# Optimization experiments

Measured on AMD Instinct MI355X. Metric: run time of the kernel, lower is better.

The kernel has to match this reference:

```python
import jax, jax.numpy as jnp
import numpy as np

B, A, D, REL, H = 8, 192, 128, 5, 128

def setup_inputs() -> dict:
    key = jax.random.key(0)
    ks = jax.random.split(key, 10)
    coord = jax.random.normal(ks[0], (B, A, D), jnp.float32)
    goal = jax.random.normal(ks[1], (B, A, D), jnp.float32)
    frontier = jax.random.normal(ks[2], (B, A, D), jnp.float32)
    rel_feat = jax.random.normal(ks[3], (B, A, A, REL), jnp.float32)
    rule_adj = jax.random.randint(ks[4], (B, A, A), 0, 2) > 0
    base_score = jax.random.normal(ks[5], (B, A, A), jnp.float32)
    graph_context = jax.random.normal(ks[6], (B, D), jnp.float32)
    fan_in = 6 * D + REL + D
    W1 = jax.random.normal(ks[7], (fan_in, H), jnp.float32) / np.sqrt(fan_in)
    b1 = jnp.zeros((H,), jnp.float32)
    W2 = jax.random.normal(ks[8], (H, 1), jnp.float32) / np.sqrt(H)
    b2 = jnp.zeros((1,), jnp.float32)
    return {"coord": coord, "goal": goal, "frontier": frontier, "rel_feat": rel_feat,
            "rule_adj": rule_adj, "base_score": base_score, "graph_context": graph_context,
            "W1": W1, "b1": b1, "W2": W2, "b2": b2}

def reference(coord, goal, frontier, rel_feat, rule_adj, base_score, graph_context, W1, b1, W2, b2):
    b, a, d = coord.shape
    def pair(x):
        xi = jnp.broadcast_to(x[:, :, None, :], (b, a, a, d))
        xj = jnp.broadcast_to(x[:, None, :, :], (b, a, a, d))
        return xi, xj
    ci, cj = pair(coord)
    gi, gj = pair(goal)
    fi, fj = pair(frontier)
    gc = jnp.broadcast_to(graph_context[:, None, None, :], (b, a, a, d))
    edge_in = jnp.concatenate([ci, cj, gi, gj, fi, fj, rel_feat, gc], axis=-1)  # [B,A,A,7D+rel]
    h = jax.nn.relu(edge_in @ W1 + b1)
    learned = (h @ W2 + b2)[..., 0]  # [B,A,A]
    score = base_score + learned
    score = jnp.where(rule_adj, score, jnp.float32(-1e9))
    weights = jax.nn.softmax(score, axis=-1)
    weights = weights * rule_adj.astype(weights.dtype)
    weights = weights / (weights.sum(axis=-1, keepdims=True) + 1e-8)
    return weights, score, learned
```

## Files before the change

kernel.cpp:

```cpp
#include <hip/hip_runtime.h>
#include <math.h>

#define NB 8
#define NA 192
#define ND 128
#define NREL 5
#define NH 128
#define ROWS 6
#define NPBLK ((NB * NA) / ROWS)

__global__ __launch_bounds__(256) void precompute_P(
    const float* __restrict__ coord, const float* __restrict__ goal,
    const float* __restrict__ frontier, const float* __restrict__ gctx,
    const float* __restrict__ W1, const float* __restrict__ b1,
    float* __restrict__ Pi, float* __restrict__ PjT, float* __restrict__ Gc)
{
    const int blk = blockIdx.x;
    const int tid = threadIdx.x;

    if (blk >= NPBLK) {
        __shared__ float red[256];
        const int b = blk - NPBLK;
        const int h = tid & 127, part = tid >> 7;
        const float* g = gctx + b * ND + part * 64;
        const float* w = W1 + (size_t)(6 * ND + NREL + part * 64) * NH + h;
        float acc = 0.f;
#pragma unroll 8
        for (int d = 0; d < 64; ++d) acc += g[d] * w[d * NH];
        red[tid] = acc;
        __syncthreads();
        if (part == 0) Gc[b * NH + h] = red[h] + red[h + 128] + b1[h];
        return;
    }

    __shared__ __align__(16) float X[ROWS][3 * ND];
    const int r0 = blk * ROWS;

    for (int idx = tid; idx < ROWS * 3 * ND; idx += 256) {
        int r = idx / (3 * ND);
        int k = idx % (3 * ND);
        int s = k >> 7, d = k & 127;
        const float* src = (s == 0) ? coord : (s == 1) ? goal : frontier;
        X[r][k] = src[(r0 + r) * ND + d];
    }
    __syncthreads();

    const int colLocal = tid & 127;
    const int role = tid >> 7;
    const int roleOff = role * 128;

    float acc[ROWS];
#pragma unroll
    for (int r = 0; r < ROWS; r++) acc[r] = 0.f;

    for (int s = 0; s < 3; ++s) {
        const float* wb = W1 + (size_t)(256 * s + roleOff) * NH + colLocal;
#pragma unroll 2
        for (int d = 0; d < ND; d += 4) {
            float w0 = wb[(d + 0) * NH];
            float w1 = wb[(d + 1) * NH];
            float w2 = wb[(d + 2) * NH];
            float w3 = wb[(d + 3) * NH];
#pragma unroll
            for (int r = 0; r < ROWS; r++) {
                float4 x = *(const float4*)&X[r][s * ND + d];
                acc[r] += x.x * w0 + x.y * w1 + x.z * w2 + x.w * w3;
            }
        }
    }

#pragma unroll
    for (int r = 0; r < ROWS; r++) {
        int row = r0 + r;
        if (role == 0) {
            Pi[(size_t)row * NH + colLocal] = acc[r];
        } else {
            int b = row / NA, a = row % NA;
            PjT[((size_t)b * NH + colLocal) * NA + a] = acc[r];
        }
    }
}

__global__ __launch_bounds__(192) void edge_kernel(
    const float* __restrict__ Pi, const float* __restrict__ PjT,
    const float* __restrict__ Gc, const float* __restrict__ W1,
    const float* __restrict__ W2, const float* __restrict__ b2v,
    const float* __restrict__ rel_feat, const int* __restrict__ rule_adj,
    const float* __restrict__ base_score,
    float* __restrict__ out_w, float* __restrict__ out_s, float* __restrict__ out_l)
{
    const int bi = blockIdx.x;
    const int b = bi / NA;
    const int tid = threadIdx.x;

    __shared__ float4 su1[NH];
    __shared__ float4 su2[NH];
    __shared__ float redA[3], redB[3], redC[3];

    if (tid < NH) {
        float pig = Pi[(size_t)bi * NH + tid] + Gc[b * NH + tid];
        const float* wr = W1 + (size_t)(6 * ND) * NH + tid;
        su1[tid] = make_float4(pig, wr[0 * NH], wr[1 * NH], wr[2 * NH]);
        su2[tid] = make_float4(wr[3 * NH], wr[4 * NH], W2[tid], 0.f);
    }

    float rel[NREL];
    const float* rf = rel_feat + ((size_t)bi * NA + tid) * NREL;
#pragma unroll
    for (int r = 0; r < NREL; r++) rel[r] = rf[r];

    __syncthreads();

    const float* pj = PjT + (size_t)b * NH * NA + tid;
    float acc = 0.f;
#pragma unroll 4
    for (int h = 0; h < NH; ++h) {
        float p = pj[h * NA];
        float4 a = su1[h];
        float4 c = su2[h];
        float pre = a.x + p;
        pre += rel[0] * a.y;
        pre += rel[1] * a.z;
        pre += rel[2] * a.w;
        pre += rel[3] * c.x;
        pre += rel[4] * c.y;
        acc += fmaxf(pre, 0.f) * c.z;
    }
    float learned = acc + b2v[0];
    out_l[(size_t)bi * NA + tid] = learned;

    const int adj = rule_adj[(size_t)bi * NA + tid];
    const float sc = adj ? (base_score[(size_t)bi * NA + tid] + learned) : -1e9f;
    out_s[(size_t)bi * NA + tid] = sc;

    const int wave = tid >> 6, lane = tid & 63;

    float m = sc;
#pragma unroll
    for (int off = 32; off > 0; off >>= 1) m = fmaxf(m, __shfl_xor(m, off, 64));
    if (lane == 0) redA[wave] = m;
    __syncthreads();
    m = fmaxf(fmaxf(redA[0], redA[1]), redA[2]);

    float e = __expf(sc - m);
    float S = e;
#pragma unroll
    for (int off = 32; off > 0; off >>= 1) S += __shfl_xor(S, off, 64);
    if (lane == 0) redB[wave] = S;
    __syncthreads();
    S = redB[0] + redB[1] + redB[2];

    float wj = adj ? e * (1.f / S) : 0.f;
    float sw = wj;
#pragma unroll
    for (int off = 32; off > 0; off >>= 1) sw += __shfl_xor(sw, off, 64);
    if (lane == 0) redC[wave] = sw;
    __syncthreads();
    sw = redC[0] + redC[1] + redC[2];

    out_w[(size_t)bi * NA + tid] = wj * (1.f / (sw + 1e-8f));
}

extern "C" void kernel_launch(void* const* d_in, const int* in_sizes, int n_in,
                              void* d_out, int out_size, void* d_ws, size_t ws_size,
                              hipStream_t stream) {
    const float* coord    = (const float*)d_in[0];
    const float* goal     = (const float*)d_in[1];
    const float* frontier = (const float*)d_in[2];
    const float* rel_feat = (const float*)d_in[3];
    const int*   rule_adj = (const int*)d_in[4];
    const float* base_sc  = (const float*)d_in[5];
    const float* gctx     = (const float*)d_in[6];
    const float* W1       = (const float*)d_in[7];
    const float* b1       = (const float*)d_in[8];
    const float* W2       = (const float*)d_in[9];
    const float* b2       = (const float*)d_in[10];

    float* Pi  = (float*)d_ws;
    float* PjT = Pi + NB * NA * NH;
    float* Gc  = PjT + NB * NH * NA;

    float* out_w = (float*)d_out;
    float* out_s = out_w + NB * NA * NA;
    float* out_l = out_s + NB * NA * NA;

    precompute_P<<<NPBLK + NB, 256, 0, stream>>>(coord, goal, frontier, gctx,
                                                 W1, b1, Pi, PjT, Gc);
    edge_kernel<<<NB * NA, 192, 0, stream>>>(Pi, PjT, Gc, W1, W2, b2, rel_feat,
                                             rule_adj, base_sc, out_w, out_s, out_l);
}
```

Measured before the change: 122.7 us.

## Split precompute K dimension across two blocks and sum partials in edge kernel

The precompute kernel now splits the 384-wide reduction over coord/goal/frontier into two halves, each handled by its own block. This doubles the block count from 256 to 512 so more of the GPU is used. The partial results are written to doubled workspace buffers and summed in the edge kernel. The cost is extra global reads in the edge kernel's inner h loop (two PjT loads per step) and twice the workspace traffic.

Result: faster. 116.8 us (-4.8%).

```diff
diff --git a/kernel.cpp b/kernel.cpp
--- a/kernel.cpp
+++ b/kernel.cpp
@@ -7,20 +7,21 @@
 #define NREL 5
 #define NH 128
 #define ROWS 6
-#define NPBLK ((NB * NA) / ROWS)
-
-__global__ __launch_bounds__(256) void precompute_P(
+#define NROWBLK ((NB * NA) / ROWS)
+#define NPBLK (NROWBLK * 2)
+
+__global__ __launch_bounds__(256, 4) void precompute_P(
     const float* __restrict__ coord, const float* __restrict__ goal,
     const float* __restrict__ frontier, const float* __restrict__ gctx,
     const float* __restrict__ W1, const float* __restrict__ b1,
-    float* __restrict__ Pi, float* __restrict__ PjT, float* __restrict__ Gc)
+    float* __restrict__ PiP, float* __restrict__ PjTP, float* __restrict__ Gc)
 {
     const int blk = blockIdx.x;
     const int tid = threadIdx.x;
 
-    if (blk >= NPBLK) {
+    if (blk >= 2 * NROWBLK) {
         __shared__ float red[256];
-        const int b = blk - NPBLK;
+        const int b = blk - 2 * NROWBLK;
         const int h = tid & 127, part = tid >> 7;
         const float* g = gctx + b * ND + part * 64;
         const float* w = W1 + (size_t)(6 * ND + NREL + part * 64) * NH + h;
@@ -33,15 +34,19 @@
         return;
     }
 
-    __shared__ __align__(16) float X[ROWS][3 * ND];
-    const int r0 = blk * ROWS;
-
-    for (int idx = tid; idx < ROWS * 3 * ND; idx += 256) {
-        int r = idx / (3 * ND);
-        int k = idx % (3 * ND);
+    const int rb = blk >> 1;
+    const int kh = blk & 1;
+    const int r0 = rb * ROWS;
+
+    __shared__ __align__(16) float X[ROWS][192];
+
+    for (int idx = tid; idx < ROWS * 192; idx += 256) {
+        int r = idx / 192;
+        int kk = idx - r * 192;
+        int k = kh * 192 + kk;
         int s = k >> 7, d = k & 127;
         const float* src = (s == 0) ? coord : (s == 1) ? goal : frontier;
-        X[r][k] = src[(r0 + r) * ND + d];
+        X[r][kk] = src[(r0 + r) * ND + d];
     }
     __syncthreads();
 
@@ -53,36 +58,39 @@
 #pragma unroll
     for (int r = 0; r < ROWS; r++) acc[r] = 0.f;
 
-    for (int s = 0; s < 3; ++s) {
-        const float* wb = W1 + (size_t)(256 * s + roleOff) * NH + colLocal;
-#pragma unroll 2
-        for (int d = 0; d < ND; d += 4) {
-            float w0 = wb[(d + 0) * NH];
-            float w1 = wb[(d + 1) * NH];
-            float w2 = wb[(d + 2) * NH];
-            float w3 = wb[(d + 3) * NH];
+    auto seg = [&](int kkStart, int sChunk, int dStart, int len) {
+        const float* wb = W1 + (size_t)(sChunk * 256 + roleOff + dStart) * NH + colLocal;
+#pragma unroll 4
+        for (int t = 0; t < len; t += 4) {
+            float w0 = wb[0 * NH];
+            float w1 = wb[1 * NH];
+            float w2 = wb[2 * NH];
+            float w3 = wb[3 * NH];
+            wb += 4 * NH;
 #pragma unroll
             for (int r = 0; r < ROWS; r++) {
-                float4 x = *(const float4*)&X[r][s * ND + d];
+                float4 x = *(const float4*)&X[r][kkStart + t];
                 acc[r] += x.x * w0 + x.y * w1 + x.z * w2 + x.w * w3;
             }
         }
-    }
+    };
+    if (kh == 0) { seg(0, 0, 0, 128); seg(128, 1, 0, 64); }
+    else         { seg(0, 1, 64, 64); seg(64, 2, 0, 128); }
 
 #pragma unroll
     for (int r = 0; r < ROWS; r++) {
         int row = r0 + r;
         if (role == 0) {
-            Pi[(size_t)row * NH + colLocal] = acc[r];
+            PiP[((size_t)kh * NB * NA + row) * NH + colLocal] = acc[r];
         } else {
-            int b = row / NA, a = row % NA;
-            PjT[((size_t)b * NH + colLocal) * NA + a] = acc[r];
+            int b = row / NA, a = row - b * NA;
+            PjTP[(((size_t)kh * NB + b) * NH + colLocal) * NA + a] = acc[r];
         }
     }
 }
 
 __global__ __launch_bounds__(192) void edge_kernel(
-    const float* __restrict__ Pi, const float* __restrict__ PjT,
+    const float* __restrict__ PiP, const float* __restrict__ PjTP,
     const float* __restrict__ Gc, const float* __restrict__ W1,
     const float* __restrict__ W2, const float* __restrict__ b2v,
     const float* __restrict__ rel_feat, const int* __restrict__ rule_adj,
@@ -98,7 +106,9 @@
     __shared__ float redA[3], redB[3], redC[3];
 
     if (tid < NH) {
-        float pig = Pi[(size_t)bi * NH + tid] + Gc[b * NH + tid];
+        float pig = PiP[(size_t)bi * NH + tid]
+                  + PiP[(size_t)(NB * NA + bi) * NH + tid]
+                  + Gc[b * NH + tid];
         const float* wr = W1 + (size_t)(6 * ND) * NH + tid;
         su1[tid] = make_float4(pig, wr[0 * NH], wr[1 * NH], wr[2 * NH]);
         su2[tid] = make_float4(wr[3 * NH], wr[4 * NH], W2[tid], 0.f);
@@ -111,11 +121,12 @@
 
     __syncthreads();
 
-    const float* pj = PjT + (size_t)b * NH * NA + tid;
+    const float* pj0 = PjTP + (size_t)b * NH * NA + tid;
+    const float* pj1 = pj0 + (size_t)NB * NH * NA;
     float acc = 0.f;
-#pragma unroll 4
+#pragma unroll 8
     for (int h = 0; h < NH; ++h) {
-        float p = pj[h * NA];
+        float p = pj0[h * NA] + pj1[h * NA];
         float4 a = su1[h];
         float4 c = su2[h];
         float pre = a.x + p;
@@ -176,16 +187,16 @@
     const float* W2       = (const float*)d_in[9];
     const float* b2       = (const float*)d_in[10];
 
-    float* Pi  = (float*)d_ws;
-    float* PjT = Pi + NB * NA * NH;
-    float* Gc  = PjT + NB * NH * NA;
+    float* PiP  = (float*)d_ws;
+    float* PjTP = PiP + 2 * NB * NA * NH;
+    float* Gc   = PjTP + 2 * NB * NH * NA;
 
     float* out_w = (float*)d_out;
     float* out_s = out_w + NB * NA * NA;
     float* out_l = out_s + NB * NA * NA;
 
-    precompute_P<<<NPBLK + NB, 256, 0, stream>>>(coord, goal, frontier, gctx,
-                                                 W1, b1, Pi, PjT, Gc);
-    edge_kernel<<<NB * NA, 192, 0, stream>>>(Pi, PjT, Gc, W1, W2, b2, rel_feat,
+    precompute_P<<<2 * NROWBLK + NB, 256, 0, stream>>>(coord, goal, frontier, gctx,
+                                                       W1, b1, PiP, PjTP, Gc);
+    edge_kernel<<<NB * NA, 192, 0, stream>>>(PiP, PjTP, Gc, W1, W2, b2, rel_feat,
                                              rule_adj, base_sc, out_w, out_s, out_l);
 }
```
